# Kernel tuning notes

Hardware: AMD Instinct MI355X
Metric: run time of the kernel (lower is better)

The kernel has to match this reference:

```python
import jax, jax.numpy as jnp
import numpy as np
import math

D = 192            # base channel dim (init arg d); s has D channels
D2 = 2 * D         # y has 2d channels
H = 48; W = 48; BS = 2
NH = 8             # attention heads (divides both D2 and D)
NY = H * W         # tokens per image


def pe2d(d_model, height, width):
    """Faithful port of positionalencoding2d: (d_model, H, W)."""
    dh = d_model // 2
    div = jnp.exp(jnp.arange(0.0, dh, 2.0) * (-math.log(10000.0) / dh))  # (dh/2,)
    pw = jnp.arange(0.0, width)[:, None] * div    # (W, dh/2)
    ph = jnp.arange(0.0, height)[:, None] * div   # (H, dh/2)
    pe = jnp.zeros((d_model, height, width), jnp.float32)
    pe = pe.at[0:dh:2].set(jnp.broadcast_to(jnp.sin(pw).T[:, None, :], (dh // 2, height, width)))
    pe = pe.at[1:dh:2].set(jnp.broadcast_to(jnp.cos(pw).T[:, None, :], (dh // 2, height, width)))
    pe = pe.at[dh::2].set(jnp.broadcast_to(jnp.sin(ph).T[:, :, None], (dh // 2, height, width)))
    pe = pe.at[dh + 1::2].set(jnp.broadcast_to(jnp.cos(ph).T[:, :, None], (dh // 2, height, width)))
    return pe


def conv1x1(x, w, b):
    # x: (b,c,h,w), w: (out,c)
    return jnp.einsum('bchw,oc->bohw', x, w) + b[None, :, None, None]


def conv3x3(x, w, b):
    out = jax.lax.conv_general_dilated(x, w, (1, 1), 'SAME',
                                       dimension_numbers=('NCHW', 'OIHW', 'NCHW'))
    return out + b[None, :, None, None]


def bn(x, g, b):
    # inference-mode batchnorm with zero-mean / unit-var running stats
    return x * g[None, :, None, None] + b[None, :, None, None]


def setup_inputs() -> dict:
    key = jax.random.key(0)
    ks = jax.random.split(key, 8)
    r = lambda k, shp: jax.random.normal(k, shp, jnp.float32) * 0.02
    return {
        'y': jax.random.normal(ks[0], (BS, D2, H, W), jnp.float32),
        's': jax.random.normal(ks[1], (BS, D, H, W), jnp.float32),
        'wq_w': r(ks[2], (D2, D2)), 'wq_b': jnp.zeros((D2,), jnp.float32),
        'wk_w': r(ks[3], (D2, D2)), 'wk_b': jnp.zeros((D2,), jnp.float32),
        'wv_w': r(ks[4], (D, D)),   'wv_b': jnp.zeros((D,), jnp.float32),
        'conv1_w': r(ks[5], (D2, D2)), 'conv1_b': jnp.zeros((D2,), jnp.float32),
        'bn1_g': jnp.ones((D2,), jnp.float32), 'bn1_b': jnp.zeros((D2,), jnp.float32),
        'conv2_w': r(ks[6], (D, D)), 'conv2_b': jnp.zeros((D,), jnp.float32),
        'bn2_g': jnp.ones((D,), jnp.float32), 'bn2_b': jnp.zeros((D,), jnp.float32),
        'up_w': r(ks[7], (D2, D2, 3, 3)), 'up_b': jnp.zeros((D2,), jnp.float32),
        'conv3_w': r(jax.random.fold_in(key, 10), (D, D2)), 'conv3_b': jnp.zeros((D,), jnp.float32),
        'bn3_g': jnp.ones((D,), jnp.float32), 'bn3_b': jnp.zeros((D,), jnp.float32),
        'sig_w': r(jax.random.fold_in(key, 11), (D, D)), 'sig_b': jnp.zeros((D,), jnp.float32),
        'bnsig_g': jnp.ones((D,), jnp.float32), 'bnsig_b': jnp.zeros((D,), jnp.float32),
    }


def reference(y, s, wq_w, wq_b, wk_w, wk_b, wv_w, wv_b,
              conv1_w, conv1_b, bn1_g, bn1_b,
              conv2_w, conv2_b, bn2_g, bn2_b,
              up_w, up_b, conv3_w, conv3_b, bn3_g, bn3_b,
              sig_w, sig_b, bnsig_g, bnsig_b):
    bs = y.shape[0]
    y = y + pe2d(D2, H, W)[None]
    s = s + pe2d(D, H, W)[None]
    # conv+BN+ReLU feature extraction
    y_c1 = jax.nn.relu(bn(conv1x1(y, conv1_w, conv1_b), bn1_g, bn1_b))
    s_c2 = jax.nn.relu(bn(conv1x1(s, conv2_w, conv2_b), bn2_g, bn2_b))
    y_c3 = conv3x3(y, up_w, up_b)                                   # 'up' branch conv
    y_c3 = jax.nn.relu(bn(conv1x1(y_c3, conv3_w, conv3_b), bn3_g, bn3_b))  # (b, D, H, W)
    # tokenize
    yt = y_c1.reshape(bs, D2, NY).transpose(0, 2, 1)   # (b, ny, 2d)
    st = s_c2.reshape(bs, D, NY).transpose(0, 2, 1)    # (b, ny, d)
    # multi-head cross attention: Q,K from y-tokens, V from s-tokens
    Q = (yt @ wq_w.T + wq_b).reshape(bs, NY, NH, D2 // NH).transpose(0, 2, 1, 3)  # (b,h,ny,2d/h)
    K = (yt @ wk_w.T + wk_b).reshape(bs, NY, NH, D2 // NH).transpose(0, 2, 1, 3)
    V = (st @ wv_w.T + wv_b).reshape(bs, NY, NH, D // NH).transpose(0, 2, 1, 3)   # (b,h,ny,d/h)
    M = jnp.einsum('bhnd,bhmd->bhnm', Q, K) / math.sqrt(D)  # scale = d**0.5 as in source
    A = jax.nn.softmax(M, axis=-1)
    Z = jnp.einsum('bhnm,bhmd->bhnd', A, V)                 # (b,h,ny,d/h)
    Z = Z.transpose(0, 2, 1, 3).reshape(bs, NY, D).transpose(0, 2, 1).reshape(bs, D, H, W)
    # sigmoid gate and fuse
    g = jax.nn.sigmoid(bn(conv1x1(Z, sig_w, sig_b), bnsig_g, bnsig_b))
    Z = g * s
    return jnp.concatenate([Z, y_c3], axis=1)               # (b, 2d, H, W)
```

## Files before the change

kernel.cpp:

```cpp
#include <hip/hip_runtime.h>
#include <hip/hip_bf16.h>

#define Dc   192
#define D2c  384
#define NYc  2304

typedef __attribute__((ext_vector_type(8))) short short8;
typedef __attribute__((ext_vector_type(4))) float f32x4;

__device__ __forceinline__ unsigned short f2bf(float f) {
    unsigned int u = __float_as_uint(f);
    u += 0x7FFFu + ((u >> 16) & 1u);
    return (unsigned short)(u >> 16);
}

__device__ __forceinline__ float pe_val(int c, int n, int C) {
    int x = n % 48, y = n / 48;
    int dh = C >> 1;
    float pos; int i;
    if (c < dh) { i = c >> 1;        pos = (float)x; }
    else        { i = (c - dh) >> 1; pos = (float)y; }
    float divv = expf((float)(2 * i) * (-9.210340371976184f / (float)dh));
    float ang = pos * divv;
    return (c & 1) ? cosf(ang) : sinf(ang);
}

__global__ __launch_bounds__(256)
void pe_y_kernel(const float* __restrict__ y, unsigned short* __restrict__ ytok) {
    int idx = blockIdx.x * 256 + threadIdx.x;
    int n = idx % NYc; int c = (idx / NYc) % D2c; int b = idx / (NYc * D2c);
    float v = y[idx] + pe_val(c, n, D2c);
    ytok[(long)b * NYc * D2c + (long)n * D2c + c] = f2bf(v);
}

__global__ __launch_bounds__(256)
void pe_s_kernel(const float* __restrict__ s, unsigned short* __restrict__ stok,
                 float* __restrict__ sch) {
    int idx = blockIdx.x * 256 + threadIdx.x;
    int n = idx % NYc; int c = (idx / NYc) % Dc; int b = idx / (NYc * Dc);
    float v = s[idx] + pe_val(c, n, Dc);
    sch[idx] = v;
    stok[(long)b * NYc * Dc + (long)n * Dc + c] = f2bf(v);
}

__global__ __launch_bounds__(256)
void cvt_w_kernel(const float* __restrict__ w0, const float* __restrict__ w1,
                  const float* __restrict__ w2, const float* __restrict__ w3,
                  const float* __restrict__ w4, const float* __restrict__ w5,
                  const float* __restrict__ w6, unsigned short* __restrict__ dst) {
    int idx = blockIdx.x * 256 + threadIdx.x;
    const float* src; int off;
    if      (idx < 147456) { src = w0; off = idx; }
    else if (idx < 294912) { src = w1; off = idx - 147456; }
    else if (idx < 442368) { src = w2; off = idx - 294912; }
    else if (idx < 479232) { src = w3; off = idx - 442368; }
    else if (idx < 516096) { src = w4; off = idx - 479232; }
    else if (idx < 552960) { src = w5; off = idx - 516096; }
    else                   { src = w6; off = idx - 552960; }
    dst[idx] = f2bf(src[off]);
}

__global__ __launch_bounds__(256)
void cvt_up_kernel(const float* __restrict__ w, unsigned short* __restrict__ wt) {
    int idx = blockIdx.x * 256 + threadIdx.x;
    int o = idx / 3456; int r = idx % 3456;
    int tap = r / 384;  int c = r % 384;
    wt[idx] = f2bf(w[((long)o * 384 + c) * 9 + tap]);
}

enum { E_BIAS = 0, E_BNRELU = 1, E_BNRELU_F32 = 2, E_SIG_F32 = 3 };

template<int EPI, bool IM2COL, bool CH_M>
__global__ __launch_bounds__(256)
void mfma_gemm(const unsigned short* __restrict__ Ar, long aBatch, int aPitch,
               const unsigned short* __restrict__ Br, long bBatch, int bPitch,
               int K,
               const float* __restrict__ bias, const float* __restrict__ bng,
               const float* __restrict__ bnb,
               const float* __restrict__ smul, long smulBatch,
               void* __restrict__ outv, long oBatch, int oPitch)
{
    int b = blockIdx.z;
    const unsigned short* A = Ar + (long)b * aBatch;
    const unsigned short* B = Br + (long)b * bBatch;
    int n0 = blockIdx.x * 64, m0 = blockIdx.y * 64;

    __shared__ __align__(16) unsigned short As[64][40];
    __shared__ __align__(16) unsigned short Bs[64][40];

    int t = threadIdx.x;
    int lane = t & 63, w = t >> 6;
    int lr = lane & 15, lg = lane >> 4;
    int wm = (w >> 1) * 32, wn = (w & 1) * 32;
    int srow = t >> 2, sc4 = t & 3;

    f32x4 zero = {0.f, 0.f, 0.f, 0.f};
    f32x4 acc[2][2] = {{zero, zero}, {zero, zero}};

    for (int k0 = 0; k0 < K; k0 += 32) {
        uint4 av, bv;
        if (!IM2COL) {
            av = *(const uint4*)(A + (long)(m0 + srow) * aPitch + k0 + sc4 * 8);
        } else {
            int tap = k0 / 384;
            int rem = k0 - tap * 384 + sc4 * 8;
            int tok = m0 + srow;
            int py = tok / 48 + tap / 3 - 1;
            int px = tok % 48 + tap % 3 - 1;
            if (py >= 0 && py < 48 && px >= 0 && px < 48)
                av = *(const uint4*)(A + (long)(py * 48 + px) * aPitch + rem);
            else
                av = make_uint4(0, 0, 0, 0);
        }
        bv = *(const uint4*)(B + (long)(n0 + srow) * bPitch + k0 + sc4 * 8);
        *(uint4*)&As[srow][sc4 * 8] = av;
        *(uint4*)&Bs[srow][sc4 * 8] = bv;
        __syncthreads();

        short8 a0 = *(const short8*)&As[wm + lr][lg * 8];
        short8 a1 = *(const short8*)&As[wm + 16 + lr][lg * 8];
        short8 b0 = *(const short8*)&Bs[wn + lr][lg * 8];
        short8 b1 = *(const short8*)&Bs[wn + 16 + lr][lg * 8];
        acc[0][0] = __builtin_amdgcn_mfma_f32_16x16x32_bf16(a0, b0, acc[0][0], 0, 0, 0);
        acc[0][1] = __builtin_amdgcn_mfma_f32_16x16x32_bf16(a0, b1, acc[0][1], 0, 0, 0);
        acc[1][0] = __builtin_amdgcn_mfma_f32_16x16x32_bf16(a1, b0, acc[1][0], 0, 0, 0);
        acc[1][1] = __builtin_amdgcn_mfma_f32_16x16x32_bf16(a1, b1, acc[1][1], 0, 0, 0);
        __syncthreads();
    }

    float* outF = (float*)outv;
    unsigned short* outH = (unsigned short*)outv;
    long ob = (long)b * oBatch;
    #pragma unroll
    for (int i = 0; i < 2; ++i)
    #pragma unroll
    for (int j = 0; j < 2; ++j)
    #pragma unroll
    for (int r = 0; r < 4; ++r) {
        int gm = m0 + wm + i * 16 + lg * 4 + r;
        int gn = n0 + wn + j * 16 + lr;
        int ch = CH_M ? gm : gn;
        float v = acc[i][j][r] + bias[ch];
        if (EPI == E_BNRELU || EPI == E_BNRELU_F32)
            v = fmaxf(fmaf(v, bng[ch], bnb[ch]), 0.f);
        if (EPI == E_SIG_F32) {
            v = fmaf(v, bng[ch], bnb[ch]);
            v = 1.f / (1.f + __expf(-v));
            v *= smul[(long)b * smulBatch + (long)gm * NYc + gn];
        }
        long o = ob + (long)gm * oPitch + gn;
        if (EPI == E_BNRELU_F32 || EPI == E_SIG_F32) outF[o] = v;
        else                                         outH[o] = f2bf(v);
    }
}

__global__ __launch_bounds__(256)
void attn_kernel(const unsigned short* __restrict__ Qt,
                 const unsigned short* __restrict__ Kt,
                 const unsigned short* __restrict__ Vc,
                 unsigned short* __restrict__ Zt)
{
    int qb = blockIdx.x;
    int bh = blockIdx.y;
    int b = bh >> 3, h = bh & 7;
    const unsigned short* Q  = Qt + (long)b * NYc * D2c + h * 48;
    const unsigned short* Kp = Kt + (long)b * NYc * D2c + h * 48;
    const unsigned short* V  = Vc + (long)b * Dc * NYc + (long)(h * 24) * NYc;
    unsigned short*       Z  = Zt + (long)b * NYc * Dc + h * 24;

    __shared__ __align__(16) unsigned short Qs[64][72];
    __shared__ __align__(16) unsigned short Ks[64][72];
    __shared__ __align__(16) unsigned short Vs[32][72];
    __shared__ __align__(16) unsigned short Ps[4][16][72];

    int t = threadIdx.x, lane = t & 63, w = t >> 6;
    int lr = lane & 15, lg = lane >> 4;
    int q0 = qb * 64;

    {
        int row = t >> 2, c4 = t & 3;
        const unsigned short* qr = Q + (long)(q0 + row) * D2c;
        *(uint4*)&Qs[row][c4 * 8] = *(const uint4*)(qr + c4 * 8);
        uint4 z = make_uint4(0, 0, 0, 0);
        uint4 v = (c4 < 2) ? *(const uint4*)(qr + 32 + c4 * 8) : z;
        *(uint4*)&Qs[row][32 + c4 * 8] = v;
    }

    float m_run[4] = {-1e30f, -1e30f, -1e30f, -1e30f};
    float l_run[4] = {0.f, 0.f, 0.f, 0.f};
    f32x4 O0 = {0.f, 0.f, 0.f, 0.f}, O1 = {0.f, 0.f, 0.f, 0.f};
    const float scale = 0.07216878364870323f;

    for (int kt = 0; kt < 36; ++kt) {
        int k0 = kt * 64;
        __syncthreads();
        {
            int row = t >> 2, c4 = t & 3;
            const unsigned short* kr = Kp + (long)(k0 + row) * D2c;
            *(uint4*)&Ks[row][c4 * 8] = *(const uint4*)(kr + c4 * 8);
            uint4 z = make_uint4(0, 0, 0, 0);
            uint4 v = (c4 < 2) ? *(const uint4*)(kr + 32 + c4 * 8) : z;
            *(uint4*)&Ks[row][32 + c4 * 8] = v;
            int vrow = t >> 3, vch = t & 7;
            uint4 vv = z;
            if (vrow < 24) vv = *(const uint4*)(V + (long)vrow * NYc + k0 + vch * 8);
            *(uint4*)&Vs[vrow][vch * 8] = vv;
        }
        __syncthreads();

        short8 aq0 = *(const short8*)&Qs[w * 16 + lr][lg * 8];
        short8 aq1 = *(const short8*)&Qs[w * 16 + lr][32 + lg * 8];
        f32x4 sS[4];
        #pragma unroll
        for (int ks = 0; ks < 4; ++ks) {
            short8 bk0 = *(const short8*)&Ks[ks * 16 + lr][lg * 8];
            short8 bk1 = *(const short8*)&Ks[ks * 16 + lr][32 + lg * 8];
            f32x4 c = {0.f, 0.f, 0.f, 0.f};
            c = __builtin_amdgcn_mfma_f32_16x16x32_bf16(aq0, bk0, c, 0, 0, 0);
            c = __builtin_amdgcn_mfma_f32_16x16x32_bf16(aq1, bk1, c, 0, 0, 0);
            sS[ks] = c;
        }

        #pragma unroll
        for (int r = 0; r < 4; ++r) {
            float s0 = sS[0][r] * scale, s1 = sS[1][r] * scale;
            float s2 = sS[2][r] * scale, s3 = sS[3][r] * scale;
            float rm = fmaxf(fmaxf(s0, s1), fmaxf(s2, s3));
            rm = fmaxf(rm, __shfl_xor(rm, 1));
            rm = fmaxf(rm, __shfl_xor(rm, 2));
            rm = fmaxf(rm, __shfl_xor(rm, 4));
            rm = fmaxf(rm, __shfl_xor(rm, 8));
            float mn = fmaxf(m_run[r], rm);
            float al = __expf(m_run[r] - mn);
            m_run[r] = mn;
            float p0 = __expf(s0 - mn), p1 = __expf(s1 - mn);
            float p2 = __expf(s2 - mn), p3 = __expf(s3 - mn);
            l_run[r] = l_run[r] * al + (p0 + p1 + p2 + p3);
            O0[r] *= al; O1[r] *= al;
            int qrow = lg * 4 + r;
            Ps[w][qrow][ 0 + lr] = f2bf(p0);
            Ps[w][qrow][16 + lr] = f2bf(p1);
            Ps[w][qrow][32 + lr] = f2bf(p2);
            Ps[w][qrow][48 + lr] = f2bf(p3);
        }

        short8 ap0 = *(const short8*)&Ps[w][lr][lg * 8];
        short8 ap1 = *(const short8*)&Ps[w][lr][32 + lg * 8];
        short8 bv00 = *(const short8*)&Vs[lr][lg * 8];
        short8 bv01 = *(const short8*)&Vs[lr][32 + lg * 8];
        short8 bv10 = *(const short8*)&Vs[16 + lr][lg * 8];
        short8 bv11 = *(const short8*)&Vs[16 + lr][32 + lg * 8];
        O0 = __builtin_amdgcn_mfma_f32_16x16x32_bf16(ap0, bv00, O0, 0, 0, 0);
        O0 = __builtin_amdgcn_mfma_f32_16x16x32_bf16(ap1, bv01, O0, 0, 0, 0);
        O1 = __builtin_amdgcn_mfma_f32_16x16x32_bf16(ap0, bv10, O1, 0, 0, 0);
        O1 = __builtin_amdgcn_mfma_f32_16x16x32_bf16(ap1, bv11, O1, 0, 0, 0);
    }

    #pragma unroll
    for (int r = 0; r < 4; ++r) {
        float l = l_run[r];
        l += __shfl_xor(l, 1);
        l += __shfl_xor(l, 2);
        l += __shfl_xor(l, 4);
        l += __shfl_xor(l, 8);
        float inv = 1.0f / l;
        int n = q0 + w * 16 + lg * 4 + r;
        unsigned short* zr = Z + (long)n * Dc;
        zr[lr] = f2bf(O0[r] * inv);
        if (lr < 8) zr[16 + lr] = f2bf(O1[r] * inv);
    }
}

extern "C" void kernel_launch(void* const* d_in, const int* in_sizes, int n_in,
                              void* d_out, int out_size, void* d_ws, size_t ws_size,
                              hipStream_t stream) {
    const float* y       = (const float*)d_in[0];
    const float* s       = (const float*)d_in[1];
    const float* wq_w    = (const float*)d_in[2];
    const float* wq_b    = (const float*)d_in[3];
    const float* wk_w    = (const float*)d_in[4];
    const float* wk_b    = (const float*)d_in[5];
    const float* wv_w    = (const float*)d_in[6];
    const float* wv_b    = (const float*)d_in[7];
    const float* conv1_w = (const float*)d_in[8];
    const float* conv1_b = (const float*)d_in[9];
    const float* bn1_g   = (const float*)d_in[10];
    const float* bn1_b   = (const float*)d_in[11];
    const float* conv2_w = (const float*)d_in[12];
    const float* conv2_b = (const float*)d_in[13];
    const float* bn2_g   = (const float*)d_in[14];
    const float* bn2_b   = (const float*)d_in[15];
    const float* up_w    = (const float*)d_in[16];
    const float* up_b    = (const float*)d_in[17];
    const float* conv3_w = (const float*)d_in[18];
    const float* conv3_b = (const float*)d_in[19];
    const float* bn3_g   = (const float*)d_in[20];
    const float* bn3_b   = (const float*)d_in[21];
    const float* sig_w   = (const float*)d_in[22];
    const float* sig_b   = (const float*)d_in[23];
    const float* bnsig_g = (const float*)d_in[24];
    const float* bnsig_b = (const float*)d_in[25];

    unsigned short* wsp = (unsigned short*)d_ws;
    unsigned short* wcvt = wsp;
    unsigned short* upwt = wcvt + 626688;
    unsigned short* y_pe = upwt + 1327104;
    unsigned short* s_pe = y_pe + 1769472;
    unsigned short* y_c1 = s_pe + 884736;
    unsigned short* s_c2 = y_c1 + 1769472;
    unsigned short* y_up = s_c2 + 884736;
    unsigned short* Qtok = y_up + 1769472;
    unsigned short* Ktok = Qtok + 1769472;
    unsigned short* Vch  = Ktok + 1769472;
    unsigned short* Ztok = Vch + 884736;
    float*          s_ch = (float*)(Ztok + 884736);

    const unsigned short* conv1wb = wcvt;
    const unsigned short* wqb     = wcvt + 147456;
    const unsigned short* wkb     = wcvt + 294912;
    const unsigned short* conv2wb = wcvt + 442368;
    const unsigned short* wvb     = wcvt + 479232;
    const unsigned short* sigwb   = wcvt + 516096;
    const unsigned short* conv3wb = wcvt + 552960;

    const long SY2 = (long)D2c * NYc;
    const long SY1 = (long)Dc * NYc;

    pe_y_kernel<<<(2 * D2c * NYc) / 256, 256, 0, stream>>>(y, y_pe);
    pe_s_kernel<<<(2 * Dc * NYc) / 256, 256, 0, stream>>>(s, s_pe, s_ch);
    cvt_w_kernel<<<626688 / 256, 256, 0, stream>>>(conv1_w, wq_w, wk_w, conv2_w,
                                                   wv_w, sig_w, conv3_w, wcvt);
    cvt_up_kernel<<<1327104 / 256, 256, 0, stream>>>(up_w, upwt);

    dim3 blk(256);
    mfma_gemm<E_BNRELU, false, false><<<dim3(6, 36, 2), blk, 0, stream>>>(
        y_pe, SY2, D2c, conv1wb, 0, D2c, D2c,
        conv1_b, bn1_g, bn1_b, nullptr, 0, y_c1, SY2, D2c);
    mfma_gemm<E_BNRELU, false, false><<<dim3(3, 36, 2), blk, 0, stream>>>(
        s_pe, SY1, Dc, conv2wb, 0, Dc, Dc,
        conv2_b, bn2_g, bn2_b, nullptr, 0, s_c2, SY1, Dc);
    mfma_gemm<E_BIAS, true, false><<<dim3(6, 36, 2), blk, 0, stream>>>(
        y_pe, SY2, D2c, upwt, 0, 9 * D2c, 9 * D2c,
        up_b, nullptr, nullptr, nullptr, 0, y_up, SY2, D2c);
    mfma_gemm<E_BNRELU_F32, false, true><<<dim3(36, 3, 2), blk, 0, stream>>>(
        conv3wb, 0, D2c, y_up, SY2, D2c, D2c,
        conv3_b, bn3_g, bn3_b, nullptr, 0,
        (float*)d_out + (long)Dc * NYc, SY2, NYc);
    mfma_gemm<E_BIAS, false, false><<<dim3(6, 36, 2), blk, 0, stream>>>(
        y_c1, SY2, D2c, wqb, 0, D2c, D2c,
        wq_b, nullptr, nullptr, nullptr, 0, Qtok, SY2, D2c);
    mfma_gemm<E_BIAS, false, false><<<dim3(6, 36, 2), blk, 0, stream>>>(
        y_c1, SY2, D2c, wkb, 0, D2c, D2c,
        wk_b, nullptr, nullptr, nullptr, 0, Ktok, SY2, D2c);
    mfma_gemm<E_BIAS, false, true><<<dim3(36, 3, 2), blk, 0, stream>>>(
        wvb, 0, Dc, s_c2, SY1, Dc, Dc,
        wv_b, nullptr, nullptr, nullptr, 0, Vch, SY1, NYc);
    attn_kernel<<<dim3(36, 16), blk, 0, stream>>>(Qtok, Ktok, Vch, Ztok);
    mfma_gemm<E_SIG_F32, false, true><<<dim3(36, 3, 2), blk, 0, stream>>>(
        sigwb, 0, Dc, Ztok, SY1, Dc, Dc,
        sig_b, bnsig_g, bnsig_b, s_ch, SY1,
        (float*)d_out, SY2, NYc);
}
```

Before: 222.6 us.

## Fuse Q/K projections, fold softmax scale into weights, split-KV attention

Q and K projections become one GEMM writing an interleaved 768-wide QK buffer, with the softmax scale times log2(e) folded into the Q weights and bias so the attention can use raw exp2. The attention kernel moves to 512 threads, where two wave halves each handle half of a 128-key tile and are merged at the end. It also adds a lazy max rescale that only fires when the running max grows by more than a threshold, plus packed bf16 conversion and a transposed S computation. Separately, the generic GEMM's K-step doubles from 32 to 64 to halve the barriers. The trade-offs are more shared memory and registers per block, and the lazy rescale lets softmax numerators reach up to 2^10 before they are rebased.

```diff
diff --git a/kernel.cpp b/kernel.cpp
--- a/kernel.cpp
+++ b/kernel.cpp
@@ -4,6 +4,8 @@
 #define Dc   192
 #define D2c  384
 #define NYc  2304
+
+#define QSCALE 0.1041175462f
 
 typedef __attribute__((ext_vector_type(8))) short short8;
 typedef __attribute__((ext_vector_type(4))) float f32x4;
@@ -12,6 +14,13 @@
     unsigned int u = __float_as_uint(f);
     u += 0x7FFFu + ((u >> 16) & 1u);
     return (unsigned short)(u >> 16);
+}
+__device__ __forceinline__ float fexp2(float x) {
+    float r; asm("v_exp_f32 %0, %1" : "=v"(r) : "v"(x)); return r;
+}
+__device__ __forceinline__ unsigned cvtpk(float lo, float hi) {
+    unsigned r; asm("v_cvt_pk_bf16_f32 %0, %1, %2" : "=v"(r) : "v"(lo), "v"(hi));
+    return r;
 }
 
 __device__ __forceinline__ float pe_val(int c, int n, int C) {
@@ -47,17 +56,21 @@
 void cvt_w_kernel(const float* __restrict__ w0, const float* __restrict__ w1,
                   const float* __restrict__ w2, const float* __restrict__ w3,
                   const float* __restrict__ w4, const float* __restrict__ w5,
-                  const float* __restrict__ w6, unsigned short* __restrict__ dst) {
+                  const float* __restrict__ w6, unsigned short* __restrict__ dst,
+                  const float* __restrict__ wq_b, const float* __restrict__ wk_b,
+                  float* __restrict__ qkb) {
     int idx = blockIdx.x * 256 + threadIdx.x;
-    const float* src; int off;
+    if (idx < 768)
+        qkb[idx] = (idx < 384) ? wq_b[idx] * QSCALE : wk_b[idx - 384];
+    const float* src; int off; float scl = 1.0f;
     if      (idx < 147456) { src = w0; off = idx; }
-    else if (idx < 294912) { src = w1; off = idx - 147456; }
+    else if (idx < 294912) { src = w1; off = idx - 147456; scl = QSCALE; }
     else if (idx < 442368) { src = w2; off = idx - 294912; }
     else if (idx < 479232) { src = w3; off = idx - 442368; }
     else if (idx < 516096) { src = w4; off = idx - 479232; }
     else if (idx < 552960) { src = w5; off = idx - 516096; }
     else                   { src = w6; off = idx - 552960; }
-    dst[idx] = f2bf(src[off]);
+    dst[idx] = f2bf(src[off] * scl);
 }
 
 __global__ __launch_bounds__(256)
@@ -85,46 +98,52 @@
     const unsigned short* B = Br + (long)b * bBatch;
     int n0 = blockIdx.x * 64, m0 = blockIdx.y * 64;
 
-    __shared__ __align__(16) unsigned short As[64][40];
-    __shared__ __align__(16) unsigned short Bs[64][40];
+    __shared__ __align__(16) unsigned short As[64][72];
+    __shared__ __align__(16) unsigned short Bs[64][72];
 
     int t = threadIdx.x;
     int lane = t & 63, w = t >> 6;
     int lr = lane & 15, lg = lane >> 4;
     int wm = (w >> 1) * 32, wn = (w & 1) * 32;
-    int srow = t >> 2, sc4 = t & 3;
 
     f32x4 zero = {0.f, 0.f, 0.f, 0.f};
     f32x4 acc[2][2] = {{zero, zero}, {zero, zero}};
 
-    for (int k0 = 0; k0 < K; k0 += 32) {
-        uint4 av, bv;
-        if (!IM2COL) {
-            av = *(const uint4*)(A + (long)(m0 + srow) * aPitch + k0 + sc4 * 8);
-        } else {
-            int tap = k0 / 384;
-            int rem = k0 - tap * 384 + sc4 * 8;
-            int tok = m0 + srow;
-            int py = tok / 48 + tap / 3 - 1;
-            int px = tok % 48 + tap % 3 - 1;
-            if (py >= 0 && py < 48 && px >= 0 && px < 48)
-                av = *(const uint4*)(A + (long)(py * 48 + px) * aPitch + rem);
-            else
-                av = make_uint4(0, 0, 0, 0);
-        }
-        bv = *(const uint4*)(B + (long)(n0 + srow) * bPitch + k0 + sc4 * 8);
-        *(uint4*)&As[srow][sc4 * 8] = av;
-        *(uint4*)&Bs[srow][sc4 * 8] = bv;
+    for (int k0 = 0; k0 < K; k0 += 64) {
+        #pragma unroll
+        for (int i = 0; i < 2; ++i) {
+            int idx = t + i * 256;
+            int row = idx >> 3, sl = idx & 7;
+            uint4 av;
+            if (!IM2COL) {
+                av = *(const uint4*)(A + (long)(m0 + row) * aPitch + k0 + sl * 8);
+            } else {
+                int gk = k0 + sl * 8;
+                int tap = gk / 384;
+                int rem = gk - tap * 384;
+                int tok = m0 + row;
+                int py = tok / 48 + tap / 3 - 1;
+                int px = tok % 48 + tap % 3 - 1;
+                av = (py >= 0 && py < 48 && px >= 0 && px < 48)
+                        ? *(const uint4*)(A + (long)(py * 48 + px) * aPitch + rem)
+                        : make_uint4(0, 0, 0, 0);
+            }
+            uint4 bv = *(const uint4*)(B + (long)(n0 + row) * bPitch + k0 + sl * 8);
+            *(uint4*)&As[row][sl * 8] = av;
+            *(uint4*)&Bs[row][sl * 8] = bv;
+        }
         __syncthreads();
-
-        short8 a0 = *(const short8*)&As[wm + lr][lg * 8];
-        short8 a1 = *(const short8*)&As[wm + 16 + lr][lg * 8];
-        short8 b0 = *(const short8*)&Bs[wn + lr][lg * 8];
-        short8 b1 = *(const short8*)&Bs[wn + 16 + lr][lg * 8];
-        acc[0][0] = __builtin_amdgcn_mfma_f32_16x16x32_bf16(a0, b0, acc[0][0], 0, 0, 0);
-        acc[0][1] = __builtin_amdgcn_mfma_f32_16x16x32_bf16(a0, b1, acc[0][1], 0, 0, 0);
-        acc[1][0] = __builtin_amdgcn_mfma_f32_16x16x32_bf16(a1, b0, acc[1][0], 0, 0, 0);
-        acc[1][1] = __builtin_amdgcn_mfma_f32_16x16x32_bf16(a1, b1, acc[1][1], 0, 0, 0);
+        #pragma unroll
+        for (int kk = 0; kk < 2; ++kk) {
+            short8 a0 = *(const short8*)&As[wm + lr][kk * 32 + lg * 8];
+            short8 a1 = *(const short8*)&As[wm + 16 + lr][kk * 32 + lg * 8];
+            short8 b0 = *(const short8*)&Bs[wn + lr][kk * 32 + lg * 8];
+            short8 b1 = *(const short8*)&Bs[wn + 16 + lr][kk * 32 + lg * 8];
+            acc[0][0] = __builtin_amdgcn_mfma_f32_16x16x32_bf16(a0, b0, acc[0][0], 0, 0, 0);
+            acc[0][1] = __builtin_amdgcn_mfma_f32_16x16x32_bf16(a0, b1, acc[0][1], 0, 0, 0);
+            acc[1][0] = __builtin_amdgcn_mfma_f32_16x16x32_bf16(a1, b0, acc[1][0], 0, 0, 0);
+            acc[1][1] = __builtin_amdgcn_mfma_f32_16x16x32_bf16(a1, b1, acc[1][1], 0, 0, 0);
+        }
         __syncthreads();
     }
 
@@ -154,120 +173,142 @@
     }
 }
 
-__global__ __launch_bounds__(256)
-void attn_kernel(const unsigned short* __restrict__ Qt,
-                 const unsigned short* __restrict__ Kt,
+__global__ __launch_bounds__(512)
+void attn_kernel(const unsigned short* __restrict__ QK,
                  const unsigned short* __restrict__ Vc,
                  unsigned short* __restrict__ Zt)
 {
     int qb = blockIdx.x;
     int bh = blockIdx.y;
     int b = bh >> 3, h = bh & 7;
-    const unsigned short* Q  = Qt + (long)b * NYc * D2c + h * 48;
-    const unsigned short* Kp = Kt + (long)b * NYc * D2c + h * 48;
-    const unsigned short* V  = Vc + (long)b * Dc * NYc + (long)(h * 24) * NYc;
+    const unsigned short* Qg = QK + (long)b * NYc * 768 + h * 48;
+    const unsigned short* Kg = Qg + 384;
+    const unsigned short* Vg = Vc + ((long)b * Dc + h * 24) * NYc;
     unsigned short*       Z  = Zt + (long)b * NYc * Dc + h * 24;
 
-    __shared__ __align__(16) unsigned short Qs[64][72];
-    __shared__ __align__(16) unsigned short Ks[64][72];
-    __shared__ __align__(16) unsigned short Vs[32][72];
-    __shared__ __align__(16) unsigned short Ps[4][16][72];
+    __shared__ __align__(16) unsigned short Ks_[128][72];
+    __shared__ __align__(16) unsigned short Vs_[32][136];
+    __shared__ __align__(16) unsigned int   Ps_[8][16][36];
 
     int t = threadIdx.x, lane = t & 63, w = t >> 6;
     int lr = lane & 15, lg = lane >> 4;
+    int tm = w >> 1, hf = w & 1;
     int q0 = qb * 64;
 
-    {
-        int row = t >> 2, c4 = t & 3;
-        const unsigned short* qr = Q + (long)(q0 + row) * D2c;
-        *(uint4*)&Qs[row][c4 * 8] = *(const uint4*)(qr + c4 * 8);
-        uint4 z = make_uint4(0, 0, 0, 0);
-        uint4 v = (c4 < 2) ? *(const uint4*)(qr + 32 + c4 * 8) : z;
-        *(uint4*)&Qs[row][32 + c4 * 8] = v;
-    }
-
-    float m_run[4] = {-1e30f, -1e30f, -1e30f, -1e30f};
-    float l_run[4] = {0.f, 0.f, 0.f, 0.f};
+    short8 z8 = {0, 0, 0, 0, 0, 0, 0, 0};
+    const unsigned short* qrow = Qg + (long)(q0 + tm * 16 + lr) * 768;
+    short8 bq0 = *(const short8*)(qrow + lg * 8);
+    short8 bq1 = (lg < 2) ? *(const short8*)(qrow + 32 + lg * 8) : z8;
+
+    float m_run = -1e30f, l_run = 0.f;
     f32x4 O0 = {0.f, 0.f, 0.f, 0.f}, O1 = {0.f, 0.f, 0.f, 0.f};
-    const float scale = 0.07216878364870323f;
-
-    for (int kt = 0; kt < 36; ++kt) {
-        int k0 = kt * 64;
+
+    for (int kt = 0; kt < 18; ++kt) {
+        long k0 = kt * 128;
+        #pragma unroll
+        for (int i = 0; i < 2; ++i) {
+            int idx = t + i * 512;
+            int row = idx >> 3, sl = idx & 7;
+            uint4 v = make_uint4(0, 0, 0, 0);
+            if (sl < 6) v = *(const uint4*)(Kg + (k0 + row) * 768 + sl * 8);
+            *(uint4*)&Ks_[row][sl * 8] = v;
+        }
+        if (t < 384) {
+            int row = t >> 4, sl = t & 15;
+            *(uint4*)&Vs_[row][sl * 8] =
+                *(const uint4*)(Vg + (long)row * NYc + k0 + sl * 8);
+        }
         __syncthreads();
-        {
-            int row = t >> 2, c4 = t & 3;
-            const unsigned short* kr = Kp + (long)(k0 + row) * D2c;
-            *(uint4*)&Ks[row][c4 * 8] = *(const uint4*)(kr + c4 * 8);
-            uint4 z = make_uint4(0, 0, 0, 0);
-            uint4 v = (c4 < 2) ? *(const uint4*)(kr + 32 + c4 * 8) : z;
-            *(uint4*)&Ks[row][32 + c4 * 8] = v;
-            int vrow = t >> 3, vch = t & 7;
-            uint4 vv = z;
-            if (vrow < 24) vv = *(const uint4*)(V + (long)vrow * NYc + k0 + vch * 8);
-            *(uint4*)&Vs[vrow][vch * 8] = vv;
-        }
-        __syncthreads();
-
-        short8 aq0 = *(const short8*)&Qs[w * 16 + lr][lg * 8];
-        short8 aq1 = *(const short8*)&Qs[w * 16 + lr][32 + lg * 8];
+
         f32x4 sS[4];
         #pragma unroll
         for (int ks = 0; ks < 4; ++ks) {
-            short8 bk0 = *(const short8*)&Ks[ks * 16 + lr][lg * 8];
-            short8 bk1 = *(const short8*)&Ks[ks * 16 + lr][32 + lg * 8];
+            short8 ak0 = *(const short8*)&Ks_[hf * 64 + ks * 16 + lr][lg * 8];
+            short8 ak1 = *(const short8*)&Ks_[hf * 64 + ks * 16 + lr][32 + lg * 8];
             f32x4 c = {0.f, 0.f, 0.f, 0.f};
-            c = __builtin_amdgcn_mfma_f32_16x16x32_bf16(aq0, bk0, c, 0, 0, 0);
-            c = __builtin_amdgcn_mfma_f32_16x16x32_bf16(aq1, bk1, c, 0, 0, 0);
+            c = __builtin_amdgcn_mfma_f32_16x16x32_bf16(ak0, bq0, c, 0, 0, 0);
+            c = __builtin_amdgcn_mfma_f32_16x16x32_bf16(ak1, bq1, c, 0, 0, 0);
             sS[ks] = c;
         }
 
-        #pragma unroll
-        for (int r = 0; r < 4; ++r) {
-            float s0 = sS[0][r] * scale, s1 = sS[1][r] * scale;
-            float s2 = sS[2][r] * scale, s3 = sS[3][r] * scale;
-            float rm = fmaxf(fmaxf(s0, s1), fmaxf(s2, s3));
-            rm = fmaxf(rm, __shfl_xor(rm, 1));
-            rm = fmaxf(rm, __shfl_xor(rm, 2));
-            rm = fmaxf(rm, __shfl_xor(rm, 4));
-            rm = fmaxf(rm, __shfl_xor(rm, 8));
-            float mn = fmaxf(m_run[r], rm);
-            float al = __expf(m_run[r] - mn);
-            m_run[r] = mn;
-            float p0 = __expf(s0 - mn), p1 = __expf(s1 - mn);
-            float p2 = __expf(s2 - mn), p3 = __expf(s3 - mn);
-            l_run[r] = l_run[r] * al + (p0 + p1 + p2 + p3);
-            O0[r] *= al; O1[r] *= al;
-            int qrow = lg * 4 + r;
-            Ps[w][qrow][ 0 + lr] = f2bf(p0);
-            Ps[w][qrow][16 + lr] = f2bf(p1);
-            Ps[w][qrow][32 + lr] = f2bf(p2);
-            Ps[w][qrow][48 + lr] = f2bf(p3);
-        }
-
-        short8 ap0 = *(const short8*)&Ps[w][lr][lg * 8];
-        short8 ap1 = *(const short8*)&Ps[w][lr][32 + lg * 8];
-        short8 bv00 = *(const short8*)&Vs[lr][lg * 8];
-        short8 bv01 = *(const short8*)&Vs[lr][32 + lg * 8];
-        short8 bv10 = *(const short8*)&Vs[16 + lr][lg * 8];
-        short8 bv11 = *(const short8*)&Vs[16 + lr][32 + lg * 8];
+        float tmax = -1e30f;
+        #pragma unroll
+        for (int ks = 0; ks < 4; ++ks)
+            #pragma unroll
+            for (int r = 0; r < 4; ++r) tmax = fmaxf(tmax, sS[ks][r]);
+        tmax = fmaxf(tmax, __shfl_xor(tmax, 16));
+        tmax = fmaxf(tmax, __shfl_xor(tmax, 32));
+
+        if (__any(tmax > m_run + 10.f)) {
+            float mn = fmaxf(m_run, tmax);
+            float al = fexp2(m_run - mn);
+            m_run = mn;
+            l_run *= al;
+            #pragma unroll
+            for (int rr = 0; rr < 4; ++rr) {
+                float arr = __shfl(al, (lane & 48) | (lg * 4 + rr));
+                O0[rr] *= arr; O1[rr] *= arr;
+            }
+        }
+
+        float psum = 0.f;
+        #pragma unroll
+        for (int ks = 0; ks < 4; ++ks) {
+            float p0 = fexp2(sS[ks][0] - m_run);
+            float p1 = fexp2(sS[ks][1] - m_run);
+            float p2 = fexp2(sS[ks][2] - m_run);
+            float p3 = fexp2(sS[ks][3] - m_run);
+            psum += (p0 + p1) + (p2 + p3);
+            Ps_[w][lr][8 * ks + 2 * lg]     = cvtpk(p0, p1);
+            Ps_[w][lr][8 * ks + 2 * lg + 1] = cvtpk(p2, p3);
+        }
+        psum += __shfl_xor(psum, 16);
+        psum += __shfl_xor(psum, 32);
+        l_run += psum;
+
+        short8 ap0 = *(const short8*)&Ps_[w][lr][4 * lg];
+        short8 ap1 = *(const short8*)&Ps_[w][lr][16 + 4 * lg];
+        short8 bv00 = *(const short8*)&Vs_[lr][hf * 64 + lg * 8];
+        short8 bv01 = *(const short8*)&Vs_[lr][hf * 64 + 32 + lg * 8];
+        short8 bv10 = *(const short8*)&Vs_[16 + lr][hf * 64 + lg * 8];
+        short8 bv11 = *(const short8*)&Vs_[16 + lr][hf * 64 + 32 + lg * 8];
         O0 = __builtin_amdgcn_mfma_f32_16x16x32_bf16(ap0, bv00, O0, 0, 0, 0);
         O0 = __builtin_amdgcn_mfma_f32_16x16x32_bf16(ap1, bv01, O0, 0, 0, 0);
         O1 = __builtin_amdgcn_mfma_f32_16x16x32_bf16(ap0, bv10, O1, 0, 0, 0);
         O1 = __builtin_amdgcn_mfma_f32_16x16x32_bf16(ap1, bv11, O1, 0, 0, 0);
+        __syncthreads();
     }
 
-    #pragma unroll
-    for (int r = 0; r < 4; ++r) {
-        float l = l_run[r];
-        l += __shfl_xor(l, 1);
-        l += __shfl_xor(l, 2);
-        l += __shfl_xor(l, 4);
-        l += __shfl_xor(l, 8);
-        float inv = 1.0f / l;
-        int n = q0 + w * 16 + lg * 4 + r;
-        unsigned short* zr = Z + (long)n * Dc;
-        zr[lr] = f2bf(O0[r] * inv);
-        if (lr < 8) zr[16 + lr] = f2bf(O1[r] * inv);
+    float* Cf = (float*)&Ps_[0][0][0];
+    float* T = Cf + tm * 576;
+    if (hf == 1) {
+        #pragma unroll
+        for (int j = 0; j < 4; ++j) {
+            T[lane * 8 + j]     = O0[j];
+            T[lane * 8 + 4 + j] = O1[j];
+        }
+        if (lane < 16) { T[512 + lane] = m_run; T[528 + lane] = l_run; }
+    }
+    __syncthreads();
+    if (hf == 0) {
+        float mB = T[512 + lr], lB = T[528 + lr];
+        float mS = fmaxf(m_run, mB);
+        float aA = fexp2(m_run - mS), aB = fexp2(mB - mS);
+        float invl = 1.f / (l_run * aA + lB * aB);
+        float fA = aA * invl, fB = aB * invl;
+        #pragma unroll
+        for (int rr = 0; rr < 4; ++rr) {
+            int src = (lane & 48) | (lg * 4 + rr);
+            float gA = __shfl(fA, src), gB = __shfl(fB, src);
+            int n = q0 + tm * 16 + lg * 4 + rr;
+            unsigned short* zr = Z + (long)n * Dc;
+            float z0 = O0[rr] * gA + T[lane * 8 + rr] * gB;
+            zr[lr] = f2bf(z0);
+            if (lr < 8) {
+                float z1 = O1[rr] * gA + T[lane * 8 + 4 + rr] * gB;
+                zr[16 + lr] = f2bf(z1);
+            }
+        }
     }
 }
 
@@ -301,23 +342,22 @@
     const float* bnsig_g = (const float*)d_in[24];
     const float* bnsig_b = (const float*)d_in[25];
 
-    unsigned short* wsp = (unsigned short*)d_ws;
-    unsigned short* wcvt = wsp;
-    unsigned short* upwt = wcvt + 626688;
-    unsigned short* y_pe = upwt + 1327104;
-    unsigned short* s_pe = y_pe + 1769472;
-    unsigned short* y_c1 = s_pe + 884736;
-    unsigned short* s_c2 = y_c1 + 1769472;
-    unsigned short* y_up = s_c2 + 884736;
-    unsigned short* Qtok = y_up + 1769472;
-    unsigned short* Ktok = Qtok + 1769472;
-    unsigned short* Vch  = Ktok + 1769472;
-    unsigned short* Ztok = Vch + 884736;
-    float*          s_ch = (float*)(Ztok + 884736);
+    unsigned short* wsp  = (unsigned short*)d_ws;
+    unsigned short* wcvt  = wsp;
+    unsigned short* upwt  = wcvt + 626688;
+    unsigned short* y_pe  = upwt + 1327104;
+    unsigned short* s_pe  = y_pe + 1769472;
+    unsigned short* y_c1  = s_pe + 884736;
+    unsigned short* s_c2  = y_c1 + 1769472;
+    unsigned short* y_up  = s_c2 + 884736;
+    unsigned short* QKtok = y_up + 1769472;
+    unsigned short* Vch   = QKtok + 3538944;
+    unsigned short* Ztok  = Vch + 884736;
+    float*          s_ch  = (float*)(Ztok + 884736);
+    float*          qkb   = s_ch + 884736;
 
     const unsigned short* conv1wb = wcvt;
-    const unsigned short* wqb     = wcvt + 147456;
-    const unsigned short* wkb     = wcvt + 294912;
+    const unsigned short* wqkb    = wcvt + 147456;
     const unsigned short* conv2wb = wcvt + 442368;
     const unsigned short* wvb     = wcvt + 479232;
     const unsigned short* sigwb   = wcvt + 516096;
@@ -329,7 +369,8 @@
     pe_y_kernel<<<(2 * D2c * NYc) / 256, 256, 0, stream>>>(y, y_pe);
     pe_s_kernel<<<(2 * Dc * NYc) / 256, 256, 0, stream>>>(s, s_pe, s_ch);
     cvt_w_kernel<<<626688 / 256, 256, 0, stream>>>(conv1_w, wq_w, wk_w, conv2_w,
-                                                   wv_w, sig_w, conv3_w, wcvt);
+                                                   wv_w, sig_w, conv3_w, wcvt,
+                                                   wq_b, wk_b, qkb);
     cvt_up_kernel<<<1327104 / 256, 256, 0, stream>>>(up_w, upwt);
 
     dim3 blk(256);
@@ -346,16 +387,13 @@
         conv3wb, 0, D2c, y_up, SY2, D2c, D2c,
         conv3_b, bn3_g, bn3_b, nullptr, 0,
         (float*)d_out + (long)Dc * NYc, SY2, NYc);
-    mfma_gemm<E_BIAS, false, false><<<dim3(6, 36, 2), blk, 0, stream>>>(
-        y_c1, SY2, D2c, wqb, 0, D2c, D2c,
-        wq_b, nullptr, nullptr, nullptr, 0, Qtok, SY2, D2c);
-    mfma_gemm<E_BIAS, false, false><<<dim3(6, 36, 2), blk, 0, stream>>>(
-        y_c1, SY2, D2c, wkb, 0, D2c, D2c,
-        wk_b, nullptr, nullptr, nullptr, 0, Ktok, SY2, D2c);
+    mfma_gemm<E_BIAS, false, false><<<dim3(12, 36, 2), blk, 0, stream>>>(
+        y_c1, SY2, D2c, wqkb, 0, D2c, D2c,
+        qkb, nullptr, nullptr, nullptr, 0, QKtok, (long)NYc * 768, 768);
     mfma_gemm<E_BIAS, false, true><<<dim3(36, 3, 2), blk, 0, stream>>>(
         wvb, 0, Dc, s_c2, SY1, Dc, Dc,
         wv_b, nullptr, nullptr, nullptr, 0, Vch, SY1, NYc);
-    attn_kernel<<<dim3(36, 16), blk, 0, stream>>>(Qtok, Ktok, Vch, Ztok);
+    attn_kernel<<<dim3(36, 16), dim3(512), 0, stream>>>(QKtok, Vch, Ztok);
     mfma_gemm<E_SIG_F32, false, true><<<dim3(36, 3, 2), blk, 0, stream>>>(
         sigwb, 0, Dc, Ztok, SY1, Dc, Dc,
         sig_b, bnsig_g, bnsig_b, s_ch, SY1,
```

Result: faster. 184.7 us (-17.0%).
